# Optimization experiments

Measured on AMD Instinct MI355X. Metric: run time of the kernel, lower is better.

## Reference

```python
import jax, jax.numpy as jnp
import numpy as np

NUM_EXPERTS = 16
HIDDEN = 2048
INTERMEDIATE = 1408
TOTAL_TOKENS = 32768  # tokens pre-sorted by expert assignment


def setup_inputs() -> dict:
    key = jax.random.key(0)
    k1, k2, k3, k4 = jax.random.split(key, 4)
    x = jax.random.normal(k1, (TOTAL_TOKENS, HIDDEN), dtype=jnp.float32)
    # normal() initializer per module; scale ~N(0, 0.02) like typical kernel_init
    w_gate = jax.random.normal(k2, (NUM_EXPERTS, HIDDEN, INTERMEDIATE), dtype=jnp.float32) * 0.02
    w_up = jax.random.normal(k3, (NUM_EXPERTS, HIDDEN, INTERMEDIATE), dtype=jnp.float32) * 0.02
    w_down = jax.random.normal(k4, (NUM_EXPERTS, INTERMEDIATE, HIDDEN), dtype=jnp.float32) * 0.02
    # tokens evenly distributed over experts; sums to TOTAL_TOKENS
    group_sizes = jnp.full((NUM_EXPERTS,), TOTAL_TOKENS // NUM_EXPERTS, dtype=jnp.int32)
    return {"x": x, "w_gate": w_gate, "w_up": w_up, "w_down": w_down,
            "group_sizes": group_sizes}


def reference(x, w_gate, w_up, w_down, group_sizes):
    # Grouped (ragged) GEMMs: rows of x are grouped contiguously by expert,
    # group_sizes[e] rows use expert e's kernel. lax.ragged_dot is the
    # idiomatic grouped-GEMM primitive (no dense [T,E] masking).
    gate = jax.lax.ragged_dot(x, w_gate, group_sizes)      # [T, I]
    up = jax.lax.ragged_dot(x, w_up, group_sizes)          # [T, I]
    h = jax.nn.silu(gate) * up                             # fused SwiGLU gating
    out = jax.lax.ragged_dot(h, w_down, group_sizes)       # [T, H]
    return out
```

## Files before the change

kernel.cpp:

```cpp
#include <hip/hip_runtime.h>
#include <hip/hip_bf16.h>

#define TOKENS 32768
#define NEXP   16
#define HID    2048
#define IMD    1408
#define BM 256
#define BK 64

typedef __bf16 bf16x8 __attribute__((ext_vector_type(8)));
typedef float  f32x4  __attribute__((ext_vector_type(4)));
typedef float  f32x16 __attribute__((ext_vector_type(16)));
typedef unsigned short u16x8 __attribute__((ext_vector_type(8)));

using gptr1_t = const __attribute__((address_space(1))) void*;
using lptr3_t = __attribute__((address_space(3))) void*;

static __device__ __forceinline__ unsigned short f2bf(float f) {
  unsigned int x = __builtin_bit_cast(unsigned int, f);
  x += 0x7fffu + ((x >> 16) & 1u);
  return (unsigned short)(x >> 16);
}
static __device__ __forceinline__ void gload16(const void* g, void* l) {
  __builtin_amdgcn_global_load_lds((gptr1_t)g, (lptr3_t)l, 16, 0, 0);
}
static __device__ __forceinline__ void vwait0() {
  asm volatile("s_waitcnt vmcnt(0)" ::: "memory");
}
static __device__ __forceinline__ void lgkm6() {
  asm volatile("s_waitcnt lgkmcnt(6)" ::: "memory");
}
static __device__ __forceinline__ void lgkm0() {
  asm volatile("s_waitcnt lgkmcnt(0)" ::: "memory");
}
static __device__ __forceinline__ f32x4 ds128(unsigned addr) {
  f32x4 d;
  asm volatile("ds_read_b128 %0, %1" : "=&v"(d) : "v"(addr));
  return d;
}

__global__ __launch_bounds__(256)
void convert_kernel(const float* __restrict__ in, unsigned short* __restrict__ out, size_t n)
{
  size_t i = ((size_t)blockIdx.x * blockDim.x + threadIdx.x) * 8;
  if (i >= n) return;
  float4 a = *(const float4*)(in + i);
  float4 b = *(const float4*)(in + i + 4);
  u16x8 o;
  o[0] = f2bf(a.x); o[1] = f2bf(a.y); o[2] = f2bf(a.z); o[3] = f2bf(a.w);
  o[4] = f2bf(b.x); o[5] = f2bf(b.y); o[6] = f2bf(b.z); o[7] = f2bf(b.w);
  *(u16x8*)(out + i) = o;
}

__global__ __launch_bounds__(256)
void transpose_conv_kernel(const float* __restrict__ in, unsigned short* __restrict__ out,
                           int K, int N)
{
  __shared__ float tile[32][33];
  const int e = blockIdx.z;
  const float* ip = in + (size_t)e * K * N;
  unsigned short* op = out + (size_t)e * K * N;
  const int c0 = blockIdx.x * 32, r0 = blockIdx.y * 32;
  const int tx = threadIdx.x, ty = threadIdx.y;
#pragma unroll
  for (int i = 0; i < 4; ++i)
    tile[ty + 8 * i][tx] = ip[(size_t)(r0 + ty + 8 * i) * N + c0 + tx];
  __syncthreads();
#pragma unroll
  for (int i = 0; i < 4; ++i)
    op[(size_t)(c0 + ty + 8 * i) * K + r0 + tx] = f2bf(tile[tx][ty + 8 * i]);
}

template<int MODE, int K, int N>
__global__ __launch_bounds__(512, 2)
void gemm_kernel(const unsigned short* __restrict__ A,
                 const unsigned short* __restrict__ B0m,
                 const unsigned short* __restrict__ B1m,
                 unsigned short* __restrict__ Hc,
                 float* __restrict__ Cf,
                 const int* __restrict__ gs)
{
  constexpr int NRT = TOKENS / BM;
  constexpr int nt  = K / BK;

  __shared__ __align__(16) unsigned short lA[2][256 * 64];
  __shared__ __align__(16) unsigned short lB[2][256 * 64];

  const int xcd = blockIdx.x & 7;
  const int i   = blockIdx.x >> 3;
  const int rt  = xcd * (NRT / 8) + (i % (NRT / 8));
  const int ct  = i / (NRT / 8);
  const int row0 = rt * BM;

  int e = 0;
  { int a0 = 0;
    for (int ii = 0; ii < NEXP; ++ii) { int s = gs[ii]; if (row0 < a0 + s) { e = ii; break; } a0 += s; } }

  const unsigned short* Ap = A + (size_t)row0 * K;
  const unsigned short* Bg = B0m + (size_t)e * N * K;
  const unsigned short* Bu = (MODE == 0) ? (B1m + (size_t)e * N * K) : nullptr;

  const int tid  = threadIdx.x;
  const int lane = tid & 63, wave = tid >> 6;
  const int wr = wave >> 2, wc = wave & 3;
  const int l31 = lane & 31, hi = lane >> 5, l7 = lane & 7;
  const int r8 = lane >> 3;
  const int slog = ((lane & 7) ^ r8) * 8;

  const unsigned sw0 = (unsigned)(((0 + hi) ^ l7) * 16);
  const unsigned sw1 = (unsigned)(((2 + hi) ^ l7) * 16);
  const unsigned sw2 = (unsigned)(((4 + hi) ^ l7) * 16);
  const unsigned sw3 = (unsigned)(((6 + hi) ^ l7) * 16);

  const unsigned lAb = (unsigned)(unsigned long long)(const void*)&lA[0][0];
  const unsigned lBb = (unsigned)(unsigned long long)(const void*)&lB[0][0];
  const unsigned aRow = lAb + (unsigned)((wr * 128 + l31) * 128);
  const unsigned bRow = lBb + (unsigned)((wc * 64 + l31) * 128);

  f32x16 acc[4][2] = {};

  auto stage = [&](int chunk, int tt) {
    const int buf = tt & 1;
    const int k0 = tt * BK;
#pragma unroll
    for (int w = 0; w < 2; ++w) {
      if (chunk >= 2) {
        const int c = chunk - 2;
        unsigned short* ldst = &lA[buf][(c * 128 + w * 64 + wave * 8) * 64];
        const int grow = c * 128 + w * 64 + wave * 8 + r8;
        gload16(Ap + (size_t)grow * K + k0 + slog, ldst);
      } else {
        unsigned short* ldst = &lB[buf][(chunk * 128 + w * 64 + wave * 8) * 64];
        const int rem = w * 64 + wave * 8 + r8;
        const int v = chunk * 128 + rem;
        if constexpr (MODE == 0) {
          const int wcq = v >> 6, p = (v >> 5) & 1, ii = v & 31;
          const unsigned short* mb = p ? Bu : Bg;
          const int gcol = ct * 128 + wcq * 32 + ii;
          gload16(mb + (size_t)gcol * K + k0 + slog, ldst);
        } else {
          const int gcol = ct * 256 + v;
          gload16(Bg + (size_t)gcol * K + k0 + slog, ldst);
        }
      }
    }
  };

  auto rdA = [&](f32x4* d, unsigned sw, unsigned bufoff) {
#pragma unroll
    for (int m = 0; m < 4; ++m)
      d[m] = ds128(aRow + bufoff + (unsigned)(m * 4096) + sw);
  };
  auto rdB = [&](f32x4* d, unsigned sw, unsigned bufoff) {
    d[0] = ds128(bRow + bufoff + sw);
    d[1] = ds128(bRow + bufoff + 4096u + sw);
  };
  auto cluster = [&](const f32x4* a4, const f32x4* b2) {
    __builtin_amdgcn_sched_barrier(0);
    __builtin_amdgcn_s_setprio(1);
#pragma unroll
    for (int m = 0; m < 4; ++m)
#pragma unroll
      for (int n2 = 0; n2 < 2; ++n2)
        acc[m][n2] = __builtin_amdgcn_mfma_f32_32x32x16_bf16(
            __builtin_bit_cast(bf16x8, a4[m]), __builtin_bit_cast(bf16x8, b2[n2]),
            acc[m][n2], 0, 0, 0);
    __builtin_amdgcn_s_setprio(0);
    __builtin_amdgcn_sched_barrier(0);
  };

  stage(0, 0); stage(1, 0); stage(2, 0); stage(3, 0);
  vwait0();
  __builtin_amdgcn_s_barrier();

  f32x4 aS0[4], bS0[2], aS1[4], bS1[2], aS2[4], bS2[2];

#pragma unroll 1
  for (int t = 0; t < nt; ++t) {
    const unsigned bufoff = (unsigned)((t & 1) * 32768);
    const bool more = (t + 1 < nt);

    rdA(aS0, sw0, bufoff); rdB(bS0, sw0, bufoff);
    rdA(aS1, sw1, bufoff); rdB(bS1, sw1, bufoff);
    lgkm6();
    cluster(aS0, bS0);
    if (more) { stage(0, t + 1); stage(1, t + 1); }
    rdA(aS2, sw2, bufoff); rdB(bS2, sw2, bufoff);
    lgkm6();
    cluster(aS1, bS1);
    if (more) { stage(2, t + 1); stage(3, t + 1); }
    rdA(aS0, sw3, bufoff); rdB(bS0, sw3, bufoff);
    lgkm6();
    cluster(aS2, bS2);
    lgkm0();
    cluster(aS0, bS0);

    vwait0();
    __builtin_amdgcn_s_barrier();
  }

#pragma unroll
  for (int m = 0; m < 4; ++m) {
    const int rowb = row0 + wr * 128 + m * 32 + 4 * hi;
    if constexpr (MODE == 0) {
      const int col = ct * 128 + wc * 32 + l31;
      f32x16 g = acc[m][0], u = acc[m][1];
#pragma unroll
      for (int r = 0; r < 16; ++r) {
        const int row = rowb + (r & 3) + 8 * (r >> 2);
        float gv = g[r];
        float s = gv / (1.f + __expf(-gv)) * u[r];
        Hc[(size_t)row * N + col] = f2bf(s);
      }
    } else {
#pragma unroll
      for (int n2 = 0; n2 < 2; ++n2) {
        const int col = ct * 256 + wc * 64 + n2 * 32 + l31;
        f32x16 v = acc[m][n2];
#pragma unroll
        for (int r = 0; r < 16; ++r) {
          const int row = rowb + (r & 3) + 8 * (r >> 2);
          Cf[(size_t)row * N + col] = v[r];
        }
      }
    }
  }
}

extern "C" void kernel_launch(void* const* d_in, const int* in_sizes, int n_in,
                              void* d_out, int out_size, void* d_ws, size_t ws_size,
                              hipStream_t stream)
{
  const float* x  = (const float*)d_in[0];
  const float* wg = (const float*)d_in[1];
  const float* wu = (const float*)d_in[2];
  const float* wd = (const float*)d_in[3];
  const int*   gs = (const int*)d_in[4];
  float* out = (float*)d_out;

  const size_t SZ_XB = (size_t)TOKENS * HID * 2;
  const size_t SZ_W  = (size_t)NEXP * HID * IMD * 2;
  const size_t SZ_H  = (size_t)TOKENS * IMD * 2;
  if (ws_size < SZ_XB + 2 * SZ_W + SZ_H) return;

  char* ws = (char*)d_ws;
  unsigned short* xb  = (unsigned short*)ws;
  unsigned short* wTg = (unsigned short*)(ws + SZ_XB);
  unsigned short* wTu = (unsigned short*)(ws + SZ_XB + SZ_W);
  unsigned short* h   = (unsigned short*)(ws + SZ_XB + 2 * SZ_W);

  const int cvt_grid = (int)(((size_t)TOKENS * HID) / (256 * 8));
  convert_kernel<<<cvt_grid, 256, 0, stream>>>(x, xb, (size_t)TOKENS * HID);

  transpose_conv_kernel<<<dim3(IMD / 32, HID / 32, NEXP), dim3(32, 8), 0, stream>>>(wg, wTg, HID, IMD);
  transpose_conv_kernel<<<dim3(IMD / 32, HID / 32, NEXP), dim3(32, 8), 0, stream>>>(wu, wTu, HID, IMD);
  gemm_kernel<0, HID, IMD><<<(TOKENS / BM) * (IMD / 128), 512, 0, stream>>>(
      xb, wTg, wTu, h, nullptr, gs);

  transpose_conv_kernel<<<dim3(HID / 32, IMD / 32, NEXP), dim3(32, 8), 0, stream>>>(wd, wTg, IMD, HID);
  gemm_kernel<1, IMD, HID><<<(TOKENS / BM) * (HID / 256), 512, 0, stream>>>(
      h, wTg, nullptr, nullptr, out, gs);
}
```

Baseline: 867.9 us.

## Switch grouped GEMM inner loop to 16x16x32 MFMA with two-phase K schedule

```diff
diff --git a/kernel.cpp b/kernel.cpp
--- a/kernel.cpp
+++ b/kernel.cpp
@@ -10,7 +10,6 @@
 
 typedef __bf16 bf16x8 __attribute__((ext_vector_type(8)));
 typedef float  f32x4  __attribute__((ext_vector_type(4)));
-typedef float  f32x16 __attribute__((ext_vector_type(16)));
 typedef unsigned short u16x8 __attribute__((ext_vector_type(8)));
 
 using gptr1_t = const __attribute__((address_space(1))) void*;
@@ -27,11 +26,12 @@
 static __device__ __forceinline__ void vwait0() {
   asm volatile("s_waitcnt vmcnt(0)" ::: "memory");
 }
-static __device__ __forceinline__ void lgkm6() {
-  asm volatile("s_waitcnt lgkmcnt(6)" ::: "memory");
-}
-static __device__ __forceinline__ void lgkm0() {
-  asm volatile("s_waitcnt lgkmcnt(0)" ::: "memory");
+static __device__ __forceinline__ void lgkm(int n) {
+  switch (n) {
+    case 0: asm volatile("s_waitcnt lgkmcnt(0)" ::: "memory"); break;
+    case 4: asm volatile("s_waitcnt lgkmcnt(4)" ::: "memory"); break;
+    default: asm volatile("s_waitcnt lgkmcnt(8)" ::: "memory"); break;
+  }
 }
 static __device__ __forceinline__ f32x4 ds128(unsigned addr) {
   f32x4 d;
@@ -103,21 +103,19 @@
   const int tid  = threadIdx.x;
   const int lane = tid & 63, wave = tid >> 6;
   const int wr = wave >> 2, wc = wave & 3;
-  const int l31 = lane & 31, hi = lane >> 5, l7 = lane & 7;
+  const int fr = lane & 15, fq = lane >> 4;
   const int r8 = lane >> 3;
   const int slog = ((lane & 7) ^ r8) * 8;
 
-  const unsigned sw0 = (unsigned)(((0 + hi) ^ l7) * 16);
-  const unsigned sw1 = (unsigned)(((2 + hi) ^ l7) * 16);
-  const unsigned sw2 = (unsigned)(((4 + hi) ^ l7) * 16);
-  const unsigned sw3 = (unsigned)(((6 + hi) ^ l7) * 16);
+  const unsigned c0 = (unsigned)(((0 + fq) ^ (fr & 7)) * 16);
+  const unsigned c1 = (unsigned)(((4 + fq) ^ (fr & 7)) * 16);
 
   const unsigned lAb = (unsigned)(unsigned long long)(const void*)&lA[0][0];
   const unsigned lBb = (unsigned)(unsigned long long)(const void*)&lB[0][0];
-  const unsigned aRow = lAb + (unsigned)((wr * 128 + l31) * 128);
-  const unsigned bRow = lBb + (unsigned)((wc * 64 + l31) * 128);
-
-  f32x16 acc[4][2] = {};
+  const unsigned aRowB = lAb + (unsigned)((wr * 128 + fr) * 128);
+  const unsigned bRowB = lBb + (unsigned)((wc * 64 + fr) * 128);
+
+  f32x4 acc[8][4] = {};
 
   auto stage = [&](int chunk, int tt) {
     const int buf = tt & 1;
@@ -146,25 +144,26 @@
     }
   };
 
-  auto rdA = [&](f32x4* d, unsigned sw, unsigned bufoff) {
+  auto rdA4 = [&](f32x4* d, int mh, unsigned c, unsigned bo) {
 #pragma unroll
     for (int m = 0; m < 4; ++m)
-      d[m] = ds128(aRow + bufoff + (unsigned)(m * 4096) + sw);
-  };
-  auto rdB = [&](f32x4* d, unsigned sw, unsigned bufoff) {
-    d[0] = ds128(bRow + bufoff + sw);
-    d[1] = ds128(bRow + bufoff + 4096u + sw);
-  };
-  auto cluster = [&](const f32x4* a4, const f32x4* b2) {
+      d[m] = ds128(aRowB + bo + (unsigned)((mh * 4 + m) * 2048) + c);
+  };
+  auto rdB4 = [&](f32x4* d, unsigned c, unsigned bo) {
+#pragma unroll
+    for (int n = 0; n < 4; ++n)
+      d[n] = ds128(bRowB + bo + (unsigned)(n * 2048) + c);
+  };
+  auto MF16 = [&](int ab, const f32x4* a4, const f32x4* b4) {
     __builtin_amdgcn_sched_barrier(0);
     __builtin_amdgcn_s_setprio(1);
 #pragma unroll
     for (int m = 0; m < 4; ++m)
 #pragma unroll
-      for (int n2 = 0; n2 < 2; ++n2)
-        acc[m][n2] = __builtin_amdgcn_mfma_f32_32x32x16_bf16(
-            __builtin_bit_cast(bf16x8, a4[m]), __builtin_bit_cast(bf16x8, b2[n2]),
-            acc[m][n2], 0, 0, 0);
+      for (int n = 0; n < 4; ++n)
+        acc[ab + m][n] = __builtin_amdgcn_mfma_f32_16x16x32_bf16(
+            __builtin_bit_cast(bf16x8, a4[m]), __builtin_bit_cast(bf16x8, b4[n]),
+            acc[ab + m][n], 0, 0, 0);
     __builtin_amdgcn_s_setprio(0);
     __builtin_amdgcn_sched_barrier(0);
   };
@@ -173,55 +172,54 @@
   vwait0();
   __builtin_amdgcn_s_barrier();
 
-  f32x4 aS0[4], bS0[2], aS1[4], bS1[2], aS2[4], bS2[2];
+  f32x4 a0[4], a1[4], b0[4], b1[4];
 
 #pragma unroll 1
   for (int t = 0; t < nt; ++t) {
-    const unsigned bufoff = (unsigned)((t & 1) * 32768);
+    const unsigned bo = (unsigned)((t & 1) * 32768);
     const bool more = (t + 1 < nt);
 
-    rdA(aS0, sw0, bufoff); rdB(bS0, sw0, bufoff);
-    rdA(aS1, sw1, bufoff); rdB(bS1, sw1, bufoff);
-    lgkm6();
-    cluster(aS0, bS0);
+    rdA4(a0, 0, c0, bo); rdB4(b0, c0, bo);
+    rdA4(a1, 1, c0, bo);
+    lgkm(4);
+    MF16(0, a0, b0);
+    rdA4(a0, 0, c1, bo); rdB4(b1, c1, bo);
+    lgkm(8);
+    MF16(4, a1, b0);
+    rdA4(a1, 1, c1, bo);
     if (more) { stage(0, t + 1); stage(1, t + 1); }
-    rdA(aS2, sw2, bufoff); rdB(bS2, sw2, bufoff);
-    lgkm6();
-    cluster(aS1, bS1);
+    lgkm(4);
+    MF16(0, a0, b1);
     if (more) { stage(2, t + 1); stage(3, t + 1); }
-    rdA(aS0, sw3, bufoff); rdB(bS0, sw3, bufoff);
-    lgkm6();
-    cluster(aS2, bS2);
-    lgkm0();
-    cluster(aS0, bS0);
+    lgkm(0);
+    MF16(4, a1, b1);
 
     vwait0();
     __builtin_amdgcn_s_barrier();
   }
 
 #pragma unroll
-  for (int m = 0; m < 4; ++m) {
-    const int rowb = row0 + wr * 128 + m * 32 + 4 * hi;
+  for (int mi = 0; mi < 8; ++mi) {
+    const int rowb = row0 + wr * 128 + ((mi >> 2) * 64) + (mi & 3) * 16 + fq * 4;
     if constexpr (MODE == 0) {
-      const int col = ct * 128 + wc * 32 + l31;
-      f32x16 g = acc[m][0], u = acc[m][1];
-#pragma unroll
-      for (int r = 0; r < 16; ++r) {
-        const int row = rowb + (r & 3) + 8 * (r >> 2);
-        float gv = g[r];
-        float s = gv / (1.f + __expf(-gv)) * u[r];
-        Hc[(size_t)row * N + col] = f2bf(s);
+#pragma unroll
+      for (int m2 = 0; m2 < 2; ++m2) {
+        const int col = ct * 128 + wc * 32 + m2 * 16 + fr;
+        f32x4 g = acc[mi][m2], u = acc[mi][m2 + 2];
+#pragma unroll
+        for (int r = 0; r < 4; ++r) {
+          float gv = g[r];
+          Hc[(size_t)(rowb + r) * N + col] = f2bf(gv / (1.f + __expf(-gv)) * u[r]);
+        }
       }
     } else {
 #pragma unroll
-      for (int n2 = 0; n2 < 2; ++n2) {
-        const int col = ct * 256 + wc * 64 + n2 * 32 + l31;
-        f32x16 v = acc[m][n2];
-#pragma unroll
-        for (int r = 0; r < 16; ++r) {
-          const int row = rowb + (r & 3) + 8 * (r >> 2);
-          Cf[(size_t)row * N + col] = v[r];
-        }
+      for (int nf = 0; nf < 4; ++nf) {
+        const int col = ct * 256 + wc * 64 + nf * 16 + fr;
+        f32x4 v = acc[mi][nf];
+#pragma unroll
+        for (int r = 0; r < 4; ++r)
+          Cf[(size_t)(rowb + r) * N + col] = v[r];
       }
     }
   }
```

Result: slower. 896.6 us (+3.3%).
